# Performance work log

Hardware: AMD Instinct MI355X
Metric: run time of the kernel (lower is better)

Reference implementation:

```python
import jax, jax.numpy as jnp
import numpy as np

B, S, DIM = 2, 2048, 4096
NH, NKV, HD = 32, 8, 128
REP = NH // NKV
ROPE_THETA = 10000.0


def _rope(x, cos, sin):
    # x: (B, S, H, HD); cos/sin: (S, HD//2). Interleaved complex rotation.
    xr, xi = x[..., 0::2], x[..., 1::2]
    c = cos[None, :, None, :]
    s = sin[None, :, None, :]
    out_r = xr * c - xi * s
    out_i = xr * s + xi * c
    return jnp.stack([out_r, out_i], axis=-1).reshape(x.shape)


def setup_inputs() -> dict:
    key = jax.random.key(0)
    k0, k1, k2, k3, k4 = jax.random.split(key, 5)
    x = jax.random.normal(k0, (B, S, DIM), jnp.float32)
    std = 0.02
    wq = jax.random.normal(k1, (NH * HD, DIM), jnp.float32) * std
    wk = jax.random.normal(k2, (NKV * HD, DIM), jnp.float32) * std
    wv = jax.random.normal(k3, (NKV * HD, DIM), jnp.float32) * std
    wo = jax.random.normal(k4, (DIM, NH * HD), jnp.float32) * std
    inv_freq = 1.0 / (ROPE_THETA ** (jnp.arange(0, HD, 2, dtype=jnp.float32) / HD))
    ang = jnp.outer(jnp.arange(S, dtype=jnp.float32), inv_freq)  # (S, HD//2)
    return {
        "x": x, "wq": wq, "wk": wk, "wv": wv, "wo": wo,
        "freqs_cos": jnp.cos(ang), "freqs_sin": jnp.sin(ang),
        "start_pos": 0,
    }


def reference(x, wq, wk, wv, wo, freqs_cos, freqs_sin, start_pos):
    bsz, seqlen, _ = x.shape
    q = (x @ wq.T).reshape(bsz, seqlen, NH, HD)
    k = (x @ wk.T).reshape(bsz, seqlen, NKV, HD)
    v = (x @ wv.T).reshape(bsz, seqlen, NKV, HD)
    q = _rope(q, freqs_cos, freqs_sin)
    k = _rope(k, freqs_cos, freqs_sin)
    # Grouped-query attention without materializing repeated KV:
    # q -> (B, NKV, REP, S, HD); k, v -> (B, NKV, S, HD)
    q = q.transpose(0, 2, 1, 3).reshape(bsz, NKV, REP, seqlen, HD)
    k = k.transpose(0, 2, 1, 3)
    v = v.transpose(0, 2, 1, 3)
    scale = 1.0 / jnp.sqrt(jnp.float32(HD))
    scores = jnp.einsum('bgrtd,bgsd->bgrts', q, k) * scale
    causal = jnp.tril(jnp.ones((seqlen, seqlen), dtype=bool))
    scores = jnp.where(causal[None, None, None], scores, jnp.finfo(scores.dtype).min)
    probs = jax.nn.softmax(scores, axis=-1)
    out = jnp.einsum('bgrts,bgsd->bgrtd', probs, v)  # (B, NKV, REP, S, HD)
    out = out.reshape(bsz, NH, seqlen, HD).transpose(0, 2, 1, 3).reshape(bsz, seqlen, NH * HD)
    return out @ wo.T
```

## Files before the change

kernel.cpp:

```cpp
#include <hip/hip_runtime.h>
#include <math.h>

#define B_    2
#define S_    2048
#define DIM_  4096
#define NH_   32
#define NKV_  8
#define HD_   128
#define MROWS (B_ * S_)
#define QDIM  (NH_ * HD_)
#define KVDIM (NKV_ * HD_)

typedef unsigned short ushort_t;
typedef __attribute__((ext_vector_type(8))) short bf16x8;
typedef __attribute__((ext_vector_type(4))) float f32x4;

#define MFMA16(a, b, c) __builtin_amdgcn_mfma_f32_16x16x32_bf16(a, b, c, 0, 0, 0)

__device__ __forceinline__ float bf2f(ushort_t u) {
  return __uint_as_float(((unsigned int)u) << 16);
}
__device__ __forceinline__ ushort_t f2bf(float f) {
  unsigned int x = __float_as_uint(f);
  return (ushort_t)((x + 0x7fffu + ((x >> 16) & 1u)) >> 16);
}
__device__ __forceinline__ void gload16(const void* g, void* l) {
  __builtin_amdgcn_global_load_lds(
      (const __attribute__((address_space(1))) void*)g,
      (__attribute__((address_space(3))) void*)l, 16, 0, 0);
}

__global__ void conv_f32_bf16(const float* __restrict__ in,
                              ushort_t* __restrict__ out) {
  int i = blockIdx.x * 256 + threadIdx.x;
  float4 a = ((const float4*)in)[i * 2 + 0];
  float4 b = ((const float4*)in)[i * 2 + 1];
  bf16x8 o;
  o[0] = (short)f2bf(a.x); o[1] = (short)f2bf(a.y);
  o[2] = (short)f2bf(a.z); o[3] = (short)f2bf(a.w);
  o[4] = (short)f2bf(b.x); o[5] = (short)f2bf(b.y);
  o[6] = (short)f2bf(b.z); o[7] = (short)f2bf(b.w);
  ((bf16x8*)out)[i] = o;
}

template <int OUT_MODE>
__global__ __launch_bounds__(256, 2) void gemm_bf16(
    const ushort_t* __restrict__ A, const ushort_t* __restrict__ W,
    void* __restrict__ Cv, int M, int N, int K) {
  constexpr int BK = 32;
  __shared__ ushort_t As[128 * BK];
  __shared__ ushort_t Ws[128 * BK];
  const int tid = threadIdx.x, lane = tid & 63, w = tid >> 6;
  const int quad = lane >> 4, l16 = lane & 15;
  const int row0 = blockIdx.y * 128, col0 = blockIdx.x * 128;
  const int wm = (w & 1) * 64, wn = (w >> 1) * 64;

  f32x4 acc[4][4] = {};

  for (int k0 = 0; k0 < K; k0 += BK) {
    __syncthreads();
#pragma unroll
    for (int i = 0; i < 2; ++i) {
      int c = i * 256 + w * 64 + lane;
      int r = c >> 2, ko = (c & 3) * 8;
      gload16(A + (size_t)(row0 + r) * K + k0 + ko,
              (char*)As + (i * 256 + w * 64) * 16);
      gload16(W + (size_t)(col0 + r) * K + k0 + ko,
              (char*)Ws + (i * 256 + w * 64) * 16);
    }
    __syncthreads();

    bf16x8 af[4], bfr[4];
#pragma unroll
    for (int mt = 0; mt < 4; ++mt)
      af[mt] = *(const bf16x8*)((char*)As + (wm + mt * 16 + l16) * 64 + quad * 16);
#pragma unroll
    for (int nt = 0; nt < 4; ++nt)
      bfr[nt] = *(const bf16x8*)((char*)Ws + (wn + nt * 16 + l16) * 64 + quad * 16);
#pragma unroll
    for (int mt = 0; mt < 4; ++mt)
#pragma unroll
      for (int nt = 0; nt < 4; ++nt)
        acc[mt][nt] = MFMA16(af[mt], bfr[nt], acc[mt][nt]);
  }

#pragma unroll
  for (int mt = 0; mt < 4; ++mt)
#pragma unroll
    for (int nt = 0; nt < 4; ++nt)
#pragma unroll
      for (int r = 0; r < 4; ++r) {
        int row = row0 + wm + mt * 16 + quad * 4 + r;
        int col = col0 + wn + nt * 16 + l16;
        float v = acc[mt][nt][r];
        if (OUT_MODE == 0)
          ((ushort_t*)Cv)[(size_t)row * N + col] = f2bf(v);
        else if (OUT_MODE == 1)
          ((float*)Cv)[(size_t)row * N + col] = v;
        else
          ((ushort_t*)Cv)[(size_t)col * M + row] = f2bf(v);
      }
}

__device__ __forceinline__ void stage_half(const ushort_t* __restrict__ src,
                                           int rowBase, int k0, char* ldsHalf,
                                           int wid, int lane, int K) {
#pragma unroll
  for (int j = 0; j < 2; ++j) {
    int ct = wid * 64 + j * 512 + lane;
    int r = ct >> 3, c = ct & 7;
    gload16(src + (size_t)(rowBase + r) * K + k0 + ((c ^ (r & 7)) << 3),
            ldsHalf + (wid * 64 + j * 512) * 16);
  }
}

__device__ __forceinline__ bf16x8 readfrag(const char* base, int row, int cc) {
  return *(const bf16x8*)(base + row * 128 + ((cc ^ (row & 7)) << 4));
}

template <int OUT_MODE>
__global__ __launch_bounds__(512, 2) void gemm256(
    const ushort_t* __restrict__ A, const ushort_t* __restrict__ W,
    void* __restrict__ Cv, int M, int N, int K) {
  __shared__ __align__(16) char lds[131072];
  const int tid = threadIdx.x, lane = tid & 63, wid = tid >> 6;
  const int quad = lane >> 4, l16 = lane & 15;
  const int wr = wid >> 2, wc = wid & 3;
  const int row0 = blockIdx.y * 256, col0 = blockIdx.x * 256;
  const int KT = K >> 6;

  f32x4 acc[8][4] = {};

  stage_half(A, row0,       0, lds,                 wid, lane, K);
  stage_half(A, row0 + 128, 0, lds + 16384,         wid, lane, K);
  stage_half(W, col0,       0, lds + 65536,         wid, lane, K);
  stage_half(W, col0 + 128, 0, lds + 65536 + 16384, wid, lane, K);
  asm volatile("s_waitcnt vmcnt(0)" ::: "memory");
  __builtin_amdgcn_s_barrier();

  for (int u = 0; u < KT; ++u) {
    char* bA = lds + (u & 1) * 32768;
    char* bB = lds + 65536 + (u & 1) * 32768;
    char* nA = lds + ((u + 1) & 1) * 32768;
    char* nB = lds + 65536 + ((u + 1) & 1) * 32768;
    const bool st = (u + 1 < KT);
    const int kn = (u + 1) << 6;

    bf16x8 bfrag[4][2];
#pragma unroll
    for (int ph = 0; ph < 4; ++ph) {
      bf16x8 afr[2][2];
#pragma unroll
      for (int mi = 0; mi < 2; ++mi)
#pragma unroll
        for (int kc = 0; kc < 2; ++kc)
          afr[mi][kc] =
              readfrag(bA, wr * 128 + (ph * 2 + mi) * 16 + l16, kc * 4 + quad);
      if (ph == 0) {
#pragma unroll
        for (int nt = 0; nt < 4; ++nt)
#pragma unroll
          for (int kc = 0; kc < 2; ++kc)
            bfrag[nt][kc] = readfrag(bB, wc * 64 + nt * 16 + l16, kc * 4 + quad);
        if (st) {
          stage_half(A, row0,       kn, nA,         wid, lane, K);
          stage_half(A, row0 + 128, kn, nA + 16384, wid, lane, K);
        }
      }
      if (ph == 1 && st) {
        stage_half(W, col0,       kn, nB,         wid, lane, K);
        stage_half(W, col0 + 128, kn, nB + 16384, wid, lane, K);
      }

      __builtin_amdgcn_s_barrier();
      asm volatile("s_waitcnt lgkmcnt(0)" ::: "memory");
      __builtin_amdgcn_sched_barrier(0);
      __builtin_amdgcn_s_setprio(1);
#pragma unroll
      for (int mi = 0; mi < 2; ++mi)
#pragma unroll
        for (int nt = 0; nt < 4; ++nt)
#pragma unroll
          for (int kc = 0; kc < 2; ++kc)
            acc[ph * 2 + mi][nt] =
                MFMA16(afr[mi][kc], bfrag[nt][kc], acc[ph * 2 + mi][nt]);
      __builtin_amdgcn_s_setprio(0);
      if (ph == 3)
        asm volatile("s_waitcnt vmcnt(0)" ::: "memory");
      __builtin_amdgcn_s_barrier();
    }
  }

#pragma unroll
  for (int mt = 0; mt < 8; ++mt)
#pragma unroll
    for (int nt = 0; nt < 4; ++nt)
#pragma unroll
      for (int r = 0; r < 4; ++r) {
        int row = row0 + wr * 128 + mt * 16 + quad * 4 + r;
        int col = col0 + wc * 64 + nt * 16 + l16;
        float v = acc[mt][nt][r];
        if (OUT_MODE == 0)
          ((ushort_t*)Cv)[(size_t)row * N + col] = f2bf(v);
        else
          ((float*)Cv)[(size_t)row * N + col] = v;
      }
}

__global__ void rope_bf16(ushort_t* __restrict__ q, ushort_t* __restrict__ k,
                          const float* __restrict__ cs,
                          const float* __restrict__ sn) {
  int idx = blockIdx.x * 256 + threadIdx.x;
  int jg = (idx & 15) * 4;
  int t = idx >> 4;
  int hh = t % (NH_ + NKV_);
  int bs = t / (NH_ + NKV_);
  int s = bs & (S_ - 1);
  float4 c4 = *(const float4*)(cs + s * 64 + jg);
  float4 s4 = *(const float4*)(sn + s * 64 + jg);
  ushort_t* p = (hh < NH_)
      ? q + (size_t)bs * QDIM + hh * HD_ + 2 * jg
      : k + (size_t)bs * KVDIM + (hh - NH_) * HD_ + 2 * jg;
  bf16x8 v = *(const bf16x8*)p;
  float cc[4] = {c4.x, c4.y, c4.z, c4.w};
  float ss[4] = {s4.x, s4.y, s4.z, s4.w};
  bf16x8 o;
#pragma unroll
  for (int u = 0; u < 4; ++u) {
    float xr = bf2f((ushort_t)v[2 * u]);
    float xi = bf2f((ushort_t)v[2 * u + 1]);
    o[2 * u]     = (short)f2bf(xr * cc[u] - xi * ss[u]);
    o[2 * u + 1] = (short)f2bf(xr * ss[u] + xi * cc[u]);
  }
  *(bf16x8*)p = o;
}

__global__ __launch_bounds__(256, 2) void attn_mfma(
    const ushort_t* __restrict__ qb, const ushort_t* __restrict__ kb,
    const ushort_t* __restrict__ vt, ushort_t* __restrict__ ob) {
  __shared__ __align__(16) char smem[2 * 16384 + 2 * 16384 + 4 * 2304];
  const int tid = threadIdx.x, lane = tid & 63, w = tid >> 6;
  const int quad = lane >> 4, l16 = lane & 15;
  char* psw = smem + 65536 + w * 2304;
  const int h = blockIdx.y, b = blockIdx.z;
  const int kvh = h >> 2;
  const float C = 0.12756113f;

  for (int half = 0; half < 2; ++half) {
    const int qt = (half == 0) ? (S_ / 64 - 1) - blockIdx.x : blockIdx.x;
    const int q0 = qt * 64;

#pragma unroll
    for (int i = 0; i < 4; ++i) {
      int r0 = w * 16 + i * 4;
      int r = r0 + (lane >> 4);
      int c = (lane & 15) ^ (r & 15);
      gload16(qb + (size_t)(b * S_ + q0 + r) * QDIM + h * HD_ + c * 8,
              smem + 16384 + r0 * 256);
      gload16(kb + (size_t)(b * S_ + r) * KVDIM + kvh * HD_ + c * 8,
              smem + r0 * 256);
      int vr0 = w * 32 + i * 8;
      int vr = vr0 + (lane >> 3);
      int vc = (lane & 7) ^ (vr & 7);
      gload16(vt + (size_t)(kvh * HD_ + vr) * MROWS + b * S_ + vc * 8,
              smem + 32768 + vr0 * 128);
    }
    __syncthreads();

    bf16x8 qf[4];
#pragma unroll
    for (int t = 0; t < 4; ++t)
      qf[t] = *(const bf16x8*)(smem + 16384 + (w * 16 + l16) * 256 +
                               (((t * 4 + quad) ^ l16) * 16));
    asm volatile("s_waitcnt lgkmcnt(0)" ::: "memory");

    float m_[4], l_[4];
    f32x4 o_[8] = {};
#pragma unroll
    for (int r = 0; r < 4; ++r) { m_[r] = -1e30f; l_[r] = 0.f; }

    for (int kt = 0; kt <= qt; ++kt) {
      char* Kc = smem + (kt & 1) * 16384;
      char* Vc = smem + 32768 + (kt & 1) * 16384;

      if (kt < qt) {
        char* Kn = smem + ((kt + 1) & 1) * 16384;
        char* Vn = smem + 32768 + ((kt + 1) & 1) * 16384;
#pragma unroll
        for (int i = 0; i < 4; ++i) {
          int r0 = w * 16 + i * 4;
          int r = r0 + (lane >> 4);
          int c = (lane & 15) ^ (r & 15);
          gload16(kb + (size_t)(b * S_ + (kt + 1) * 64 + r) * KVDIM + kvh * HD_ + c * 8,
                  Kn + r0 * 256);
          int vr0 = w * 32 + i * 8;
          int vr = vr0 + (lane >> 3);
          int vc = (lane & 7) ^ (vr & 7);
          gload16(vt + (size_t)(kvh * HD_ + vr) * MROWS + b * S_ + (kt + 1) * 64 + vc * 8,
                  Vn + vr0 * 128);
        }
      }

      const int ntmax = (kt == qt) ? w : 3;
      f32x4 s[4];
      __builtin_amdgcn_s_setprio(1);
#pragma unroll
      for (int nt = 0; nt < 4; ++nt) {
        if (nt <= ntmax) {
          f32x4 a = {0.f, 0.f, 0.f, 0.f};
#pragma unroll
          for (int t = 0; t < 4; ++t) {
            bf16x8 kf = *(const bf16x8*)(Kc + (nt * 16 + l16) * 256 +
                                         (((t * 4 + quad) ^ l16) * 16));
            a = MFMA16(qf[t], kf, a);
          }
          s[nt] = a;
        } else {
          s[nt] = (f32x4){-INFINITY, -INFINITY, -INFINITY, -INFINITY};
        }
      }
      __builtin_amdgcn_s_setprio(0);

      float p[4][4], al[4];
#pragma unroll
      for (int r = 0; r < 4; ++r) {
        float v[4];
#pragma unroll
        for (int nt = 0; nt < 4; ++nt) {
          float vv = s[nt][r] * C;
          if (kt == qt && nt == w && l16 > quad * 4 + r) vv = -INFINITY;
          v[nt] = vv;
        }
        float mx = fmaxf(fmaxf(v[0], v[1]), fmaxf(v[2], v[3]));
#pragma unroll
        for (int d = 1; d < 16; d <<= 1) mx = fmaxf(mx, __shfl_xor(mx, d, 64));
        float mnew = fmaxf(m_[r], mx);
        float a0 = __builtin_amdgcn_exp2f(m_[r] - mnew);
        float sum = 0.f;
#pragma unroll
        for (int nt = 0; nt < 4; ++nt) {
          p[nt][r] = __builtin_amdgcn_exp2f(v[nt] - mnew);
          sum += p[nt][r];
        }
#pragma unroll
        for (int d = 1; d < 16; d <<= 1) sum += __shfl_xor(sum, d, 64);
        l_[r] = l_[r] * a0 + sum;
        m_[r] = mnew;
        al[r] = a0;
      }

#pragma unroll
      for (int r = 0; r < 4; ++r)
#pragma unroll
        for (int nt = 0; nt < 4; ++nt)
          ((ushort_t*)psw)[(quad * 4 + r) * 72 + nt * 16 + l16] = f2bf(p[nt][r]);

#pragma unroll
      for (int dt = 0; dt < 8; ++dt)
#pragma unroll
        for (int r = 0; r < 4; ++r) o_[dt][r] *= al[r];

      asm volatile("s_waitcnt lgkmcnt(0)" ::: "memory");
      bf16x8 pf[2];
#pragma unroll
      for (int kc = 0; kc < 2; ++kc)
        pf[kc] = *(const bf16x8*)(psw + l16 * 144 + kc * 64 + quad * 16);

      __builtin_amdgcn_s_setprio(1);
#pragma unroll
      for (int dt = 0; dt < 8; ++dt) {
#pragma unroll
        for (int kc = 0; kc < 2; ++kc) {
          bf16x8 vf = *(const bf16x8*)(Vc + (dt * 16 + l16) * 128 +
                                       (((kc * 4 + quad) ^ (l16 & 7)) * 16));
          o_[dt] = MFMA16(pf[kc], vf, o_[dt]);
        }
      }
      __builtin_amdgcn_s_setprio(0);

      __syncthreads();
    }

#pragma unroll
    for (int r = 0; r < 4; ++r) {
      float linv = 1.0f / l_[r];
      size_t base = (size_t)(b * S_ + q0 + w * 16 + quad * 4 + r) * QDIM + h * HD_;
#pragma unroll
      for (int dt = 0; dt < 8; ++dt)
        ob[base + dt * 16 + l16] = f2bf(o_[dt][r] * linv);
    }
  }
}

extern "C" void kernel_launch(void* const* d_in, const int* in_sizes, int n_in,
                              void* d_out, int out_size, void* d_ws, size_t ws_size,
                              hipStream_t stream) {
  const float* x  = (const float*)d_in[0];
  const float* wq = (const float*)d_in[1];
  const float* wk = (const float*)d_in[2];
  const float* wv = (const float*)d_in[3];
  const float* wo = (const float*)d_in[4];
  const float* fc = (const float*)d_in[5];
  const float* fs = (const float*)d_in[6];
  float* out = (float*)d_out;

  char* ws = (char*)d_ws;
  ushort_t* xb    = (ushort_t*)(ws);
  ushort_t* wqb   = (ushort_t*)(ws + (32ull << 20));
  ushort_t* wkb   = (ushort_t*)(ws + (64ull << 20));
  ushort_t* wvb   = (ushort_t*)(ws + (72ull << 20));
  ushort_t* qbuf  = (ushort_t*)(ws + (80ull << 20));
  ushort_t* kbuf  = (ushort_t*)(ws + (112ull << 20));
  ushort_t* vtb   = (ushort_t*)(ws + (120ull << 20));
  ushort_t* attnb = (ushort_t*)(ws + (128ull << 20));
  ushort_t* wob   = xb;

  dim3 blk(256);
  dim3 blk512(512);

  conv_f32_bf16<<<(MROWS * DIM_) / 2048, blk, 0, stream>>>(x, xb);
  conv_f32_bf16<<<(QDIM * DIM_) / 2048, blk, 0, stream>>>(wq, wqb);
  conv_f32_bf16<<<(KVDIM * DIM_) / 2048, blk, 0, stream>>>(wk, wkb);
  conv_f32_bf16<<<(KVDIM * DIM_) / 2048, blk, 0, stream>>>(wv, wvb);

  gemm256<0><<<dim3(QDIM / 256, MROWS / 256), blk512, 0, stream>>>(xb, wqb, qbuf, MROWS, QDIM, DIM_);
  gemm_bf16<0><<<dim3(KVDIM / 128, MROWS / 128), blk, 0, stream>>>(xb, wkb, kbuf, MROWS, KVDIM, DIM_);
  gemm_bf16<2><<<dim3(KVDIM / 128, MROWS / 128), blk, 0, stream>>>(xb, wvb, vtb, MROWS, KVDIM, DIM_);

  rope_bf16<<<(MROWS * (NH_ + NKV_) * 16) / 256, blk, 0, stream>>>(qbuf, kbuf, fc, fs);

  attn_mfma<<<dim3(S_ / 128, NH_, B_), blk, 0, stream>>>(qbuf, kbuf, vtb, attnb);

  conv_f32_bf16<<<(QDIM * DIM_) / 2048, blk, 0, stream>>>(wo, wob);
  gemm256<1><<<dim3(QDIM / 256, MROWS / 256), blk512, 0, stream>>>(attnb, wob, out, MROWS, QDIM, DIM_);
}
```

Baseline: 787.3 us.

## Single-buffer attention K/V tiles for higher occupancy and use DPP reductions

The attention kernel drops K/V double buffering in LDS, shrinking shared memory from about 74KB to about 42KB and raising launch bounds to 3 blocks per CU. Each key tile is now loaded synchronously at the top of the iteration, with barriers before and after the load. Q is staged through the K buffer. The 16-lane max and sum reductions in softmax switch from shfl_xor to DPP row operations. The aim is to hide load latency through more resident waves instead of explicit prefetch, at the risk of exposing load latency and tightening the register budget.

```diff
diff --git a/kernel.cpp b/kernel.cpp
--- a/kernel.cpp
+++ b/kernel.cpp
@@ -28,6 +28,26 @@
   __builtin_amdgcn_global_load_lds(
       (const __attribute__((address_space(1))) void*)g,
       (__attribute__((address_space(3))) void*)l, 16, 0, 0);
+}
+
+template <int CTRL>
+__device__ __forceinline__ float dpp_f(float x) {
+  return __int_as_float(__builtin_amdgcn_update_dpp(
+      0, __float_as_int(x), CTRL, 0xF, 0xF, true));
+}
+__device__ __forceinline__ float dpp_max16(float x) {
+  x = fmaxf(x, dpp_f<0xB1>(x));
+  x = fmaxf(x, dpp_f<0x4E>(x));
+  x = fmaxf(x, dpp_f<0x141>(x));
+  x = fmaxf(x, dpp_f<0x140>(x));
+  return x;
+}
+__device__ __forceinline__ float dpp_sum16(float x) {
+  x += dpp_f<0xB1>(x);
+  x += dpp_f<0x4E>(x);
+  x += dpp_f<0x141>(x);
+  x += dpp_f<0x140>(x);
+  return x;
 }
 
 __global__ void conv_f32_bf16(const float* __restrict__ in,
@@ -235,13 +255,15 @@
   *(bf16x8*)p = o;
 }
 
-__global__ __launch_bounds__(256, 2) void attn_mfma(
+__global__ __launch_bounds__(256, 3) void attn_mfma(
     const ushort_t* __restrict__ qb, const ushort_t* __restrict__ kb,
     const ushort_t* __restrict__ vt, ushort_t* __restrict__ ob) {
-  __shared__ __align__(16) char smem[2 * 16384 + 2 * 16384 + 4 * 2304];
+  __shared__ __align__(16) char smem[16384 + 16384 + 4 * 2304];
+  char* Ks = smem;
+  char* Vs = smem + 16384;
   const int tid = threadIdx.x, lane = tid & 63, w = tid >> 6;
   const int quad = lane >> 4, l16 = lane & 15;
-  char* psw = smem + 65536 + w * 2304;
+  char* psw = smem + 32768 + w * 2304;
   const int h = blockIdx.y, b = blockIdx.z;
   const int kvh = h >> 2;
   const float C = 0.12756113f;
@@ -250,27 +272,20 @@
     const int qt = (half == 0) ? (S_ / 64 - 1) - blockIdx.x : blockIdx.x;
     const int q0 = qt * 64;
 
+    __syncthreads();
 #pragma unroll
     for (int i = 0; i < 4; ++i) {
       int r0 = w * 16 + i * 4;
       int r = r0 + (lane >> 4);
       int c = (lane & 15) ^ (r & 15);
       gload16(qb + (size_t)(b * S_ + q0 + r) * QDIM + h * HD_ + c * 8,
-              smem + 16384 + r0 * 256);
-      gload16(kb + (size_t)(b * S_ + r) * KVDIM + kvh * HD_ + c * 8,
-              smem + r0 * 256);
-      int vr0 = w * 32 + i * 8;
-      int vr = vr0 + (lane >> 3);
-      int vc = (lane & 7) ^ (vr & 7);
-      gload16(vt + (size_t)(kvh * HD_ + vr) * MROWS + b * S_ + vc * 8,
-              smem + 32768 + vr0 * 128);
+              Ks + r0 * 256);
     }
     __syncthreads();
-
     bf16x8 qf[4];
 #pragma unroll
     for (int t = 0; t < 4; ++t)
-      qf[t] = *(const bf16x8*)(smem + 16384 + (w * 16 + l16) * 256 +
+      qf[t] = *(const bf16x8*)(Ks + (w * 16 + l16) * 256 +
                                (((t * 4 + quad) ^ l16) * 16));
     asm volatile("s_waitcnt lgkmcnt(0)" ::: "memory");
 
@@ -280,26 +295,21 @@
     for (int r = 0; r < 4; ++r) { m_[r] = -1e30f; l_[r] = 0.f; }
 
     for (int kt = 0; kt <= qt; ++kt) {
-      char* Kc = smem + (kt & 1) * 16384;
-      char* Vc = smem + 32768 + (kt & 1) * 16384;
-
-      if (kt < qt) {
-        char* Kn = smem + ((kt + 1) & 1) * 16384;
-        char* Vn = smem + 32768 + ((kt + 1) & 1) * 16384;
-#pragma unroll
-        for (int i = 0; i < 4; ++i) {
-          int r0 = w * 16 + i * 4;
-          int r = r0 + (lane >> 4);
-          int c = (lane & 15) ^ (r & 15);
-          gload16(kb + (size_t)(b * S_ + (kt + 1) * 64 + r) * KVDIM + kvh * HD_ + c * 8,
-                  Kn + r0 * 256);
-          int vr0 = w * 32 + i * 8;
-          int vr = vr0 + (lane >> 3);
-          int vc = (lane & 7) ^ (vr & 7);
-          gload16(vt + (size_t)(kvh * HD_ + vr) * MROWS + b * S_ + (kt + 1) * 64 + vc * 8,
-                  Vn + vr0 * 128);
-        }
-      }
+      __syncthreads();
+#pragma unroll
+      for (int i = 0; i < 4; ++i) {
+        int r0 = w * 16 + i * 4;
+        int r = r0 + (lane >> 4);
+        int c = (lane & 15) ^ (r & 15);
+        gload16(kb + (size_t)(b * S_ + kt * 64 + r) * KVDIM + kvh * HD_ + c * 8,
+                Ks + r0 * 256);
+        int vr0 = w * 32 + i * 8;
+        int vr = vr0 + (lane >> 3);
+        int vc = (lane & 7) ^ (vr & 7);
+        gload16(vt + (size_t)(kvh * HD_ + vr) * MROWS + b * S_ + kt * 64 + vc * 8,
+                Vs + vr0 * 128);
+      }
+      __syncthreads();
 
       const int ntmax = (kt == qt) ? w : 3;
       f32x4 s[4];
@@ -310,7 +320,7 @@
           f32x4 a = {0.f, 0.f, 0.f, 0.f};
 #pragma unroll
           for (int t = 0; t < 4; ++t) {
-            bf16x8 kf = *(const bf16x8*)(Kc + (nt * 16 + l16) * 256 +
+            bf16x8 kf = *(const bf16x8*)(Ks + (nt * 16 + l16) * 256 +
                                          (((t * 4 + quad) ^ l16) * 16));
             a = MFMA16(qf[t], kf, a);
           }
@@ -332,8 +342,7 @@
           v[nt] = vv;
         }
         float mx = fmaxf(fmaxf(v[0], v[1]), fmaxf(v[2], v[3]));
-#pragma unroll
-        for (int d = 1; d < 16; d <<= 1) mx = fmaxf(mx, __shfl_xor(mx, d, 64));
+        mx = dpp_max16(mx);
         float mnew = fmaxf(m_[r], mx);
         float a0 = __builtin_amdgcn_exp2f(m_[r] - mnew);
         float sum = 0.f;
@@ -342,8 +351,7 @@
           p[nt][r] = __builtin_amdgcn_exp2f(v[nt] - mnew);
           sum += p[nt][r];
         }
-#pragma unroll
-        for (int d = 1; d < 16; d <<= 1) sum += __shfl_xor(sum, d, 64);
+        sum = dpp_sum16(sum);
         l_[r] = l_[r] * a0 + sum;
         m_[r] = mnew;
         al[r] = a0;
@@ -371,14 +379,12 @@
       for (int dt = 0; dt < 8; ++dt) {
 #pragma unroll
         for (int kc = 0; kc < 2; ++kc) {
-          bf16x8 vf = *(const bf16x8*)(Vc + (dt * 16 + l16) * 128 +
+          bf16x8 vf = *(const bf16x8*)(Vs + (dt * 16 + l16) * 128 +
                                        (((kc * 4 + quad) ^ (l16 & 7)) * 16));
           o_[dt] = MFMA16(pf[kc], vf, o_[dt]);
         }
       }
       __builtin_amdgcn_s_setprio(0);
-
-      __syncthreads();
     }
 
 #pragma unroll
```

New measurement: 765.1 us. 1.03x faster.
